# Kernel optimization log

Measured on AMD Instinct MI355X. Metric: run time of the kernel, lower is better.

The kernel has to match this reference:

```python
import jax, jax.numpy as jnp
import numpy as np

B, C_IN, H, W = 32, 64, 32, 32
C_OUT, KH, KW = 128, 3, 3
STRIDE, PAD = 1, 1
ALPHA, R, N_IDEAL, VT, V_D = 0.0005625, 0.1, 1.5, 0.025, 0.1


def setup_inputs() -> dict:
    key = jax.random.key(0)
    k1, k2 = jax.random.split(key)
    input_voltage = jax.random.normal(k1, (B, C_IN, H, W), dtype=jnp.float32)
    # theta = randn * 2 + 4, per the torch module
    theta = jax.random.normal(k2, (C_OUT, C_IN, KH, KW), dtype=jnp.float32) * 2.0 + 4.0
    return {"input_voltage": input_voltage, "theta": theta}


def _unfold(x):
    # Equivalent of F.unfold: -> [B, outHW, C_in, KH*KW] (torch channel-major ordering)
    out_h = (H + 2 * PAD - KH) // STRIDE + 1
    out_w = (W + 2 * PAD - KW) // STRIDE + 1
    xp = jnp.pad(x, ((0, 0), (0, 0), (PAD, PAD), (PAD, PAD)))
    # small fixed loop over the KH*KW kernel offsets
    patches = jnp.stack(
        [xp[:, :, di:di + out_h * STRIDE:STRIDE, dj:dj + out_w * STRIDE:STRIDE]
         for di in range(KH) for dj in range(KW)],
        axis=2,
    )  # [B, C_in, KH*KW, out_h, out_w]
    unf = patches.reshape(B, C_IN, KH * KW, out_h * out_w)
    return jnp.transpose(unf, (0, 3, 1, 2)), out_h, out_w  # [B, outHW, C_in, kk]


def _forward(input_voltage, theta):
    unfolded, out_h, out_w = _unfold(input_voltage)  # [B, P, C, kk]
    theta_flat = theta.reshape(C_OUT, C_IN, KH * KW)
    inv_denom = 1.0 / (2.0 * N_IDEAL * VT)
    shift = V_D * inv_denom

    def per_channel(carry, theta_k):  # theta_k: [C_in, kk]
        z = (unfolded - theta_k[None, None, :, :]) * inv_denom  # [B, P, C, kk]
        t1 = jax.nn.softplus(z) ** 2          # log(1+exp(.))^2, numerically stable
        t2 = jax.nn.softplus(z - shift) ** 2
        return carry, (t1 - t2).sum(axis=(2, 3))  # [B, P]

    _, I = jax.lax.scan(per_channel, 0, theta_flat)  # [C_out, B, P]
    out = ALPHA * R * jnp.transpose(I, (1, 0, 2))    # [B, C_out, P]
    out = out.reshape(B, C_OUT, out_h, out_w)
    return jnp.clip(out, 0.0, 9.0)


def reference(input_voltage, theta):
    return _forward(input_voltage, theta)
```

## Files before the change

kernel.cpp:

```cpp
#include <hip/hip_runtime.h>
#include <math.h>
#include <stdint.h>

#define BB    32
#define CIN   64
#define HH    32
#define WW    32
#define COUT  128
#define PP    1024
#define OTILE 4
#define PTILE 256
#define NPAD  12
#define TABN  2048
#define TROW  36
#define TWSZ  148

static constexpr float  MSC8     = 153.88747102815611f;
static constexpr double M2Nd     = 0.26359713811572677;
static constexpr float  OUTSCALE = 2.7025482032898827e-05f;
static constexpr float  ZLO      = -3.0f;
static constexpr float  TABH     = 0.125f;
static constexpr float  IDXBIAS  = 24.0f;
static constexpr float  CUTBIAS  = 4.0f;

__global__ __launch_bounds__(256) void sort_theta_kernel(
    const float* __restrict__ theta, uint2* __restrict__ ws)
{
    int gid = blockIdx.x * 256 + threadIdx.x;
    if (gid >= COUT * CIN) return;
    int o = gid >> 6, c = gid & 63;
    const float* tg = theta + (size_t)gid * 9;
    float    tv[NPAD];
    uint32_t kv[NPAD];
#pragma unroll
    for (int k = 0; k < 9; ++k) {
        tv[k] = fmaf(tg[k], -MSC8, IDXBIAS);
        int dy = k / 3, dx = k - 3 * dy;
        kv[k] = (uint32_t)((dy * TROW + dx) * 4);
    }
    for (int i = 1; i < 9; ++i) {
        float    key = tv[i];
        uint32_t kk  = kv[i];
        int j = i - 1;
        while (j >= 0 && tv[j] < key) { tv[j + 1] = tv[j]; kv[j + 1] = kv[j]; --j; }
        tv[j + 1] = key; kv[j + 1] = kk;
    }
    tv[9] = -1e30f; kv[9] = 0;
    tv[10] = -1e30f; kv[10] = 0;
    tv[11] = -1e30f; kv[11] = 0;
    uint2* og = ws + (size_t)(c * COUT + o) * NPAD;
#pragma unroll
    for (int j = 0; j < NPAD; ++j) og[j] = make_uint2(__float_as_uint(tv[j]), kv[j]);
}

__global__ __launch_bounds__(256) void bandcut_kernel(
    const float* __restrict__ x, float* __restrict__ bandcut)
{
    int t  = threadIdx.x;
    int bc = blockIdx.x;
    const float4* xp = (const float4*)(x + (size_t)bc * PP);
    float4 v = xp[t];
    float m = fmaxf(fmaxf(v.x, v.y), fmaxf(v.z, v.w));
    m = fmaxf(m, __shfl_xor(m, 1));
    m = fmaxf(m, __shfl_xor(m, 2));
    m = fmaxf(m, __shfl_xor(m, 4));
    __shared__ float rmax[32];
    if ((t & 7) == 0) rmax[t >> 3] = m;
    __syncthreads();
    if (t < 16) {
        int r0 = max(2 * t - 1, 0), r3 = min(2 * t + 2, 31);
        float mm = rmax[r0];
        for (int r = r0 + 1; r <= r3; ++r) mm = fmaxf(mm, rmax[r]);
        mm = fmaxf(mm, 0.0f);
        int b = bc >> 6, c = bc & 63;
        bandcut[((b * 16 + t) << 6) + c] = fmaf(mm, -MSC8, CUTBIAS);
    }
}

__global__ __launch_bounds__(256) void ftable_kernel(float2* __restrict__ tab)
{
    int i = blockIdx.x * 256 + threadIdx.x;
    if (i >= TABN) return;
    if (i == 0) { tab[0] = make_float2(0.0f, 0.0f); return; }
    double Z0 = (double)ZLO + (double)TABH * i;
    double Z1 = Z0 + (double)TABH;
    auto fd = [](double Z) {
        double E = exp2(Z);
        double a = log2(1.0 + E);
        double b = log2(1.0 + E * M2Nd);
        return a * a - b * b;
    };
    double y0 = fd(Z0), y1 = fd(Z1);
    double c1 = y1 - y0;
    double c0 = y0 - (double)i * c1;
    tab[i] = make_float2((float)c0, (float)c1);
}

__global__ __launch_bounds__(256) void nlconv_kernel(
    const float* __restrict__ x,
    const uint2* __restrict__ wst,
    const float* __restrict__ wcut,
    const float2* __restrict__ ftabg,
    float* __restrict__ out)
{
    __shared__ float  sxi[4 * TWSZ];
    __shared__ float2 ftab[TABN];

    const int t  = threadIdx.x;
    const int b  = blockIdx.x;
    const int pt = blockIdx.y;
    const int ot = blockIdx.z;
    const int w  = t >> 6;
    const int l  = t & 63;
    const int o0 = ot * OTILE;
    const int band = pt * 4 + w;
    const int rl = l >> 5, col = l & 31;

#pragma unroll
    for (int k = 0; k < TABN / 256; ++k) ftab[t + 256 * k] = ftabg[t + 256 * k];

    const int wbase = w * TWSZ;
    int   gofs[3];
    float msc[3];
    int   laddr[3];
#pragma unroll
    for (int i = 0; i < 3; ++i) {
        int e  = l + 64 * i;
        bool valid = (e < 144);
        int ec = valid ? e : 144;
        int r  = ec / TROW;
        int tc = ec - r * TROW;
        int grow = band * 2 - 1 + r;
        int gcol = tc - 1;
        bool inter = valid && (grow >= 0) && (grow < HH) && (gcol >= 0) && (gcol < WW) && (r < 4);
        gofs[i]  = (min(max(grow, 0), HH - 1) << 5) + min(max(gcol, 0), WW - 1);
        msc[i]   = inter ? MSC8 : 0.0f;
        laddr[i] = wbase + min(ec, TWSZ - 1);
    }

    const float vcut = wcut[(size_t)((b * 16 + band) << 6) + l];

    const int sp1 = (l >> 3) * NPAD + (l & 7);
    const int sp2 = (l & 7) * NPAD + 8;

    const float* xc0 = x + (size_t)b * CIN * PP;
    const uint2* wso = wst + (size_t)o0 * NPAD;
    const char*  sxb = (const char*)sxi + ((wbase + rl * TROW + col) << 2);

    float acc[OTILE];
#pragma unroll
    for (int i = 0; i < OTILE; ++i) acc[i] = 0.0f;

    float xv[3];
#pragma unroll
    for (int i = 0; i < 3; ++i) xv[i] = xc0[gofs[i]] * msc[i];
    float f1 = __uint_as_float(wso[sp1].x);
    float f2 = __uint_as_float(wso[sp2].x);
#pragma unroll
    for (int i = 0; i < 3; ++i) sxi[laddr[i]] = xv[i];
#pragma unroll
    for (int i = 0; i < 3; ++i) xv[i] = xc0[PP + gofs[i]] * msc[i];

    __syncthreads();

    for (int c = 0; c < CIN; ++c) {
        const float cutp = __uint_as_float(
            (uint32_t)__builtin_amdgcn_readlane((int)__float_as_uint(vcut), c));
        unsigned long long mA = __ballot(f1 > cutp);
        unsigned long long mB = __ballot(f2 > cutp);

        {
            int cn = min(c + 1, CIN - 1);
            const uint2* wsn = wso + (size_t)cn * (COUT * NPAD);
            f1 = __uint_as_float(wsn[sp1].x);
            f2 = __uint_as_float(wsn[sp2].x);
        }

        const uint2* thc = wso + (size_t)c * (COUT * NPAD);

#pragma unroll
        for (int g = 0; g < OTILE; ++g) {
            int cnt = (int)__popcll(mA & (0xFFull << (8 * g)))
                    + (int)((mB >> g) & 1ull);
            int np = (cnt + 1) >> 1;
            asm volatile("" : "+s"(np));
            const uint2* gth = thc + g * NPAD;
            uint4 pc = *(const uint4*)gth;
            float a = acc[g];
#pragma unroll 1
            for (int j = 0; j < np; ++j) {
                uint4 pn = *(const uint4*)(gth + 2 * j + 2);
                {
                    float xa = *(const float*)(sxb + pc.y);
                    float u  = xa + __uint_as_float(pc.x);
                    uint32_t i;
                    asm("v_cvt_u32_f32_e32 %0, %1" : "=v"(i) : "v"(u));
                    float2 cf = ftab[i];
                    a = fmaf(cf.y, u, a) + cf.x;
                }
                {
                    float xa = *(const float*)(sxb + pc.w);
                    float u  = xa + __uint_as_float(pc.z);
                    uint32_t i;
                    asm("v_cvt_u32_f32_e32 %0, %1" : "=v"(i) : "v"(u));
                    float2 cf = ftab[i];
                    a = fmaf(cf.y, u, a) + cf.x;
                }
                pc = pn;
            }
            acc[g] = a;
        }

#pragma unroll
        for (int i = 0; i < 3; ++i) sxi[laddr[i]] = xv[i];
        {
            int c2 = min(c + 2, CIN - 1);
            const float* xcn = xc0 + (size_t)c2 * PP;
#pragma unroll
            for (int i = 0; i < 3; ++i) xv[i] = xcn[gofs[i]] * msc[i];
        }
    }

    float* ob = out + ((size_t)b * COUT + o0) * PP + pt * PTILE + t;
#pragma unroll
    for (int o = 0; o < OTILE; ++o) {
        float v = acc[o] * OUTSCALE;
        v = fminf(fmaxf(v, 0.0f), 9.0f);
        ob[(size_t)o * PP] = v;
    }
}

extern "C" void kernel_launch(void* const* d_in, const int* in_sizes, int n_in,
                              void* d_out, int out_size, void* d_ws, size_t ws_size,
                              hipStream_t stream) {
    const float* x     = (const float*)d_in[0];
    const float* theta = (const float*)d_in[1];
    float* out         = (float*)d_out;

    uint2*  ws_theta = (uint2*)d_ws;
    float*  ws_cut   = (float*)(ws_theta + (size_t)CIN * COUT * NPAD + 2);
    float2* ws_tab   = (float2*)(ws_cut + (size_t)BB * 16 * 64);

    sort_theta_kernel<<<dim3((COUT * CIN + 255) / 256), dim3(256), 0, stream>>>(theta, ws_theta);
    bandcut_kernel<<<dim3(BB * CIN), dim3(256), 0, stream>>>(x, ws_cut);
    ftable_kernel<<<dim3(TABN / 256), dim3(256), 0, stream>>>(ws_tab);

    dim3 grid(BB, PP / PTILE, COUT / OTILE);
    nlconv_kernel<<<grid, dim3(256), 0, stream>>>(x, ws_theta, ws_cut, ws_tab, out);
}
```

Measured before the change: 267.0 us.

## Replace sorted-theta band-cut skipping with dense unrolled 9-tap evaluation

Drops the theta sorting kernel and the per-band input max kernel, along with the ballot and popcount early-exit loop over sorted taps. Every channel now evaluates all nine taps per output channel in a fully unrolled loop, with the input taps held in registers and two independent accumulators. The aim is to trade skipped work for branch-free, latency-friendly straight-line code and fewer launches. This risks doing more table lookups when the cutoff would have skipped most taps.

```diff
diff --git a/kernel.cpp b/kernel.cpp
--- a/kernel.cpp
+++ b/kernel.cpp
@@ -10,7 +10,7 @@
 #define PP    1024
 #define OTILE 4
 #define PTILE 256
-#define NPAD  12
+#define TPAD  12
 #define TABN  2048
 #define TROW  36
 #define TWSZ  148
@@ -21,60 +21,18 @@
 static constexpr float  ZLO      = -3.0f;
 static constexpr float  TABH     = 0.125f;
 static constexpr float  IDXBIAS  = 24.0f;
-static constexpr float  CUTBIAS  = 4.0f;
 
-__global__ __launch_bounds__(256) void sort_theta_kernel(
-    const float* __restrict__ theta, uint2* __restrict__ ws)
+__global__ __launch_bounds__(256) void thp_kernel(
+    const float* __restrict__ theta, float* __restrict__ ws)
 {
     int gid = blockIdx.x * 256 + threadIdx.x;
     if (gid >= COUT * CIN) return;
     int o = gid >> 6, c = gid & 63;
     const float* tg = theta + (size_t)gid * 9;
-    float    tv[NPAD];
-    uint32_t kv[NPAD];
+    float* og = ws + (size_t)(c * COUT + o) * TPAD;
 #pragma unroll
-    for (int k = 0; k < 9; ++k) {
-        tv[k] = fmaf(tg[k], -MSC8, IDXBIAS);
-        int dy = k / 3, dx = k - 3 * dy;
-        kv[k] = (uint32_t)((dy * TROW + dx) * 4);
-    }
-    for (int i = 1; i < 9; ++i) {
-        float    key = tv[i];
-        uint32_t kk  = kv[i];
-        int j = i - 1;
-        while (j >= 0 && tv[j] < key) { tv[j + 1] = tv[j]; kv[j + 1] = kv[j]; --j; }
-        tv[j + 1] = key; kv[j + 1] = kk;
-    }
-    tv[9] = -1e30f; kv[9] = 0;
-    tv[10] = -1e30f; kv[10] = 0;
-    tv[11] = -1e30f; kv[11] = 0;
-    uint2* og = ws + (size_t)(c * COUT + o) * NPAD;
-#pragma unroll
-    for (int j = 0; j < NPAD; ++j) og[j] = make_uint2(__float_as_uint(tv[j]), kv[j]);
-}
-
-__global__ __launch_bounds__(256) void bandcut_kernel(
-    const float* __restrict__ x, float* __restrict__ bandcut)
-{
-    int t  = threadIdx.x;
-    int bc = blockIdx.x;
-    const float4* xp = (const float4*)(x + (size_t)bc * PP);
-    float4 v = xp[t];
-    float m = fmaxf(fmaxf(v.x, v.y), fmaxf(v.z, v.w));
-    m = fmaxf(m, __shfl_xor(m, 1));
-    m = fmaxf(m, __shfl_xor(m, 2));
-    m = fmaxf(m, __shfl_xor(m, 4));
-    __shared__ float rmax[32];
-    if ((t & 7) == 0) rmax[t >> 3] = m;
-    __syncthreads();
-    if (t < 16) {
-        int r0 = max(2 * t - 1, 0), r3 = min(2 * t + 2, 31);
-        float mm = rmax[r0];
-        for (int r = r0 + 1; r <= r3; ++r) mm = fmaxf(mm, rmax[r]);
-        mm = fmaxf(mm, 0.0f);
-        int b = bc >> 6, c = bc & 63;
-        bandcut[((b * 16 + t) << 6) + c] = fmaf(mm, -MSC8, CUTBIAS);
-    }
+    for (int k = 0; k < 9; ++k) og[k] = fmaf(tg[k], -MSC8, IDXBIAS);
+    og[9] = -1e30f; og[10] = -1e30f; og[11] = -1e30f;
 }
 
 __global__ __launch_bounds__(256) void ftable_kernel(float2* __restrict__ tab)
@@ -98,8 +56,7 @@
 
 __global__ __launch_bounds__(256) void nlconv_kernel(
     const float* __restrict__ x,
-    const uint2* __restrict__ wst,
-    const float* __restrict__ wcut,
+    const float* __restrict__ wth,
     const float2* __restrict__ ftabg,
     float* __restrict__ out)
 {
@@ -138,24 +95,19 @@
         laddr[i] = wbase + min(ec, TWSZ - 1);
     }
 
-    const float vcut = wcut[(size_t)((b * 16 + band) << 6) + l];
+    const float* xc0 = x + (size_t)b * CIN * PP;
+    const int xb = wbase + rl * TROW + col;
 
-    const int sp1 = (l >> 3) * NPAD + (l & 7);
-    const int sp2 = (l & 7) * NPAD + 8;
+    constexpr int KOFS[9] = {0, 1, 2, TROW, TROW + 1, TROW + 2,
+                             2 * TROW, 2 * TROW + 1, 2 * TROW + 2};
 
-    const float* xc0 = x + (size_t)b * CIN * PP;
-    const uint2* wso = wst + (size_t)o0 * NPAD;
-    const char*  sxb = (const char*)sxi + ((wbase + rl * TROW + col) << 2);
-
-    float acc[OTILE];
+    float accA[OTILE], accB[OTILE];
 #pragma unroll
-    for (int i = 0; i < OTILE; ++i) acc[i] = 0.0f;
+    for (int i = 0; i < OTILE; ++i) { accA[i] = 0.0f; accB[i] = 0.0f; }
 
     float xv[3];
 #pragma unroll
     for (int i = 0; i < 3; ++i) xv[i] = xc0[gofs[i]] * msc[i];
-    float f1 = __uint_as_float(wso[sp1].x);
-    float f2 = __uint_as_float(wso[sp2].x);
 #pragma unroll
     for (int i = 0; i < 3; ++i) sxi[laddr[i]] = xv[i];
 #pragma unroll
@@ -164,67 +116,45 @@
     __syncthreads();
 
     for (int c = 0; c < CIN; ++c) {
-        const float cutp = __uint_as_float(
-            (uint32_t)__builtin_amdgcn_readlane((int)__float_as_uint(vcut), c));
-        unsigned long long mA = __ballot(f1 > cutp);
-        unsigned long long mB = __ballot(f2 > cutp);
-
-        {
-            int cn = min(c + 1, CIN - 1);
-            const uint2* wsn = wso + (size_t)cn * (COUT * NPAD);
-            f1 = __uint_as_float(wsn[sp1].x);
-            f2 = __uint_as_float(wsn[sp2].x);
-        }
-
-        const uint2* thc = wso + (size_t)c * (COUT * NPAD);
-
+        float xn[9];
 #pragma unroll
-        for (int g = 0; g < OTILE; ++g) {
-            int cnt = (int)__popcll(mA & (0xFFull << (8 * g)))
-                    + (int)((mB >> g) & 1ull);
-            int np = (cnt + 1) >> 1;
-            asm volatile("" : "+s"(np));
-            const uint2* gth = thc + g * NPAD;
-            uint4 pc = *(const uint4*)gth;
-            float a = acc[g];
-#pragma unroll 1
-            for (int j = 0; j < np; ++j) {
-                uint4 pn = *(const uint4*)(gth + 2 * j + 2);
-                {
-                    float xa = *(const float*)(sxb + pc.y);
-                    float u  = xa + __uint_as_float(pc.x);
-                    uint32_t i;
-                    asm("v_cvt_u32_f32_e32 %0, %1" : "=v"(i) : "v"(u));
-                    float2 cf = ftab[i];
-                    a = fmaf(cf.y, u, a) + cf.x;
-                }
-                {
-                    float xa = *(const float*)(sxb + pc.w);
-                    float u  = xa + __uint_as_float(pc.z);
-                    uint32_t i;
-                    asm("v_cvt_u32_f32_e32 %0, %1" : "=v"(i) : "v"(u));
-                    float2 cf = ftab[i];
-                    a = fmaf(cf.y, u, a) + cf.x;
-                }
-                pc = pn;
-            }
-            acc[g] = a;
-        }
+        for (int k = 0; k < 9; ++k) xn[k] = sxi[xb + KOFS[k]];
 
 #pragma unroll
         for (int i = 0; i < 3; ++i) sxi[laddr[i]] = xv[i];
+
         {
             int c2 = min(c + 2, CIN - 1);
             const float* xcn = xc0 + (size_t)c2 * PP;
 #pragma unroll
             for (int i = 0; i < 3; ++i) xv[i] = xcn[gofs[i]] * msc[i];
         }
+
+        const float* thc = wth + ((size_t)c * COUT + o0) * TPAD;
+#pragma unroll
+        for (int g = 0; g < OTILE; ++g) {
+            const float* tg9 = thc + g * TPAD;
+            float tv[9];
+#pragma unroll
+            for (int k = 0; k < 9; ++k) tv[k] = tg9[k];
+            float a0 = accA[g], a1 = accB[g];
+#pragma unroll
+            for (int k = 0; k < 9; ++k) {
+                float u = xn[k] + tv[k];
+                uint32_t i;
+                asm("v_cvt_u32_f32_e32 %0, %1" : "=v"(i) : "v"(u));
+                float2 cf = ftab[i];
+                a0 += cf.x;
+                a1 = fmaf(cf.y, u, a1);
+            }
+            accA[g] = a0; accB[g] = a1;
+        }
     }
 
     float* ob = out + ((size_t)b * COUT + o0) * PP + pt * PTILE + t;
 #pragma unroll
     for (int o = 0; o < OTILE; ++o) {
-        float v = acc[o] * OUTSCALE;
+        float v = (accA[o] + accB[o]) * OUTSCALE;
         v = fminf(fmaxf(v, 0.0f), 9.0f);
         ob[(size_t)o * PP] = v;
     }
@@ -237,14 +167,12 @@
     const float* theta = (const float*)d_in[1];
     float* out         = (float*)d_out;
 
-    uint2*  ws_theta = (uint2*)d_ws;
-    float*  ws_cut   = (float*)(ws_theta + (size_t)CIN * COUT * NPAD + 2);
-    float2* ws_tab   = (float2*)(ws_cut + (size_t)BB * 16 * 64);
+    float*  ws_thp = (float*)d_ws;
+    float2* ws_tab = (float2*)(ws_thp + (size_t)CIN * COUT * TPAD);
 
-    sort_theta_kernel<<<dim3((COUT * CIN + 255) / 256), dim3(256), 0, stream>>>(theta, ws_theta);
-    bandcut_kernel<<<dim3(BB * CIN), dim3(256), 0, stream>>>(x, ws_cut);
+    thp_kernel<<<dim3((COUT * CIN + 255) / 256), dim3(256), 0, stream>>>(theta, ws_thp);
     ftable_kernel<<<dim3(TABN / 256), dim3(256), 0, stream>>>(ws_tab);
 
     dim3 grid(BB, PP / PTILE, COUT / OTILE);
-    nlconv_kernel<<<grid, dim3(256), 0, stream>>>(x, ws_theta, ws_cut, ws_tab, out);
+    nlconv_kernel<<<grid, dim3(256), 0, stream>>>(x, ws_thp, ws_tab, out);
 }
```

New measurement: 456.2 us. +70.8%, slower.
